# Kernel tuning notes

Hardware: AMD Instinct MI355X
Metric: run time of the kernel (lower is better)

Reference implementation:

```python
import jax, jax.numpy as jnp
import numpy as np

N, M = 20000, 5000
D_IN, D_OUT = 256, 512
EPS = 1e-5


def setup_inputs() -> dict:
    key = jax.random.key(0)
    k1, k2, k3, k4 = jax.random.split(key, 4)
    x = jax.random.normal(k1, (N, D_IN), dtype=jnp.float32)
    H = (jax.random.uniform(k2, (N, M)) < 0.05).astype(jnp.float32)
    W_node = jax.random.normal(k3, (D_IN, D_OUT), dtype=jnp.float32) / np.sqrt(D_IN)
    W_res = jax.random.normal(k4, (D_IN, D_OUT), dtype=jnp.float32) / np.sqrt(D_IN)
    gamma = jnp.ones((D_OUT,), dtype=jnp.float32)
    beta = jnp.zeros((D_OUT,), dtype=jnp.float32)
    return {"x": x, "H": H, "W_node": W_node, "W_res": W_res, "gamma": gamma, "beta": beta}


def reference(x, H, W_node, W_res, gamma, beta):
    # degrees, clamped to >= 1
    d_v = jnp.clip(jnp.sum(H, axis=1), 1.0)   # [N] node degree
    d_e = jnp.clip(jnp.sum(H, axis=0), 1.0)   # [M] hyperedge degree
    x_proj = x @ W_node                       # [N, d_out]
    edge_feat = (H.T @ x_proj) / d_e[:, None] # [M, d_out] node -> edge aggregation
    node_update = (H @ edge_feat) / d_v[:, None]  # [N, d_out] edge -> node
    h = node_update + x @ W_res               # residual (d_in != d_out -> linear)
    # LayerNorm over last dim
    mu = jnp.mean(h, axis=-1, keepdims=True)
    var = jnp.mean(jnp.square(h - mu), axis=-1, keepdims=True)
    out = (h - mu) * jax.lax.rsqrt(var + EPS) * gamma + beta
    return out  # dropout is identity at inference
```

## Files before the change

### kernel.cpp

```cpp
#include <hip/hip_runtime.h>


#define N_NODES 20000
#define M_EDGES 5000
#define MPAD    5120
#define NPAD    20480
#define NW      320
#define MW      80
#define DIN     256
#define DOUT    512
#define SPLITS  16

typedef short bf16x4 __attribute__((ext_vector_type(4)));
typedef short bf16x8 __attribute__((ext_vector_type(8)));
typedef float f32x4 __attribute__((ext_vector_type(4)));
typedef unsigned long long u64;

#define MFMA16(A, B, C) __builtin_amdgcn_mfma_f32_16x16x32_bf16((A), (B), (C), 0, 0, 0)

__device__ __forceinline__ unsigned short f2b(float f) {
  unsigned u = __builtin_bit_cast(unsigned, f);
  return (unsigned short)((u + 0x7FFFu + ((u >> 16) & 1u)) >> 16);
}

__device__ __forceinline__ void stage16(const void* g, void* l) {
  __builtin_amdgcn_global_load_lds(
      (const __attribute__((address_space(1))) unsigned int*)g,
      (__attribute__((address_space(3))) unsigned int*)l, 16, 0, 0);
}

__device__ __forceinline__ bf16x8 expand8(unsigned b) {
  union { unsigned u[4]; bf16x8 v; } r;
  const unsigned t = b | (b << 15);
  r.u[0] = (t & 0x00010001u) * 0x3F80u;
  r.u[1] = ((t >> 2) & 0x00010001u) * 0x3F80u;
  r.u[2] = ((t >> 4) & 0x00010001u) * 0x3F80u;
  r.u[3] = ((t >> 6) & 0x00010001u) * 0x3F80u;
  return r.v;
}

__global__ __launch_bounds__(256) void prep_kernel(const float* __restrict__ Wn,
                                                   const float* __restrict__ Wr,
                                                   unsigned short* __restrict__ WT) {
  const int q = blockIdx.x * 256 + threadIdx.x;
  const int j = q >> 9, k = q & 511;
  const float v = (k < 256) ? Wn[(size_t)k * 512 + j] : Wr[(size_t)(k - 256) * 512 + j];
  WT[(size_t)j * 512 + k] = f2b(v);
}

__global__ __launch_bounds__(256) void xt_kernel(const float* __restrict__ x,
                                                 unsigned short* __restrict__ xpb) {
  const int j = threadIdx.x;
  const int n8 = blockIdx.x;
  union { unsigned u[4]; bf16x8 v; } o;
#pragma unroll
  for (int p = 0; p < 4; ++p) {
    const int n = n8 * 8 + 2 * p;
    const float v0 = (n < N_NODES) ? x[(size_t)n * DIN + j] : 0.f;
    const float v1 = (n + 1 < N_NODES) ? x[(size_t)(n + 1) * DIN + j] : 0.f;
    o.u[p] = (unsigned)f2b(v0) | ((unsigned)f2b(v1) << 16);
  }
  *(bf16x8*)(xpb + ((size_t)n8 * 256 + j) * 8) = o.v;
}

__global__ __launch_bounds__(256) void pack_kernel(const float* __restrict__ H,
                                                   u64* __restrict__ Hb,
                                                   u64* __restrict__ HTb) {
  const int t = threadIdx.x;
  const int l = t & 63;
  const int w = t >> 6;
  const int g = blockIdx.x;
  const int h = blockIdx.y;
  const int n0 = g * 64;
  const int mc = h * 1024 + 4 * t;
  u64 ht0 = 0, ht1 = 0, ht2 = 0, ht3 = 0;
  const int mw = h * 16 + w * 4 + (l >> 4);
  u64* hbp = Hb + (size_t)mw * NPAD + n0;
  const bool hbw = ((l & 15) == 0);
  const int shn = 4 * (l & 15);

  for (int r = 0; r < 64; ++r) {
    const int n = n0 + r;
    unsigned nib = 0;
    if (n < N_NODES) {
      if (mc + 3 < M_EDGES) {
        const float4 v = *(const float4*)(H + (size_t)n * M_EDGES + mc);
        nib = (v.x != 0.f ? 1u : 0u) | (v.y != 0.f ? 2u : 0u) |
              (v.z != 0.f ? 4u : 0u) | (v.w != 0.f ? 8u : 0u);
      } else if (mc < M_EDGES) {
#pragma unroll
        for (int j = 0; j < 4; ++j)
          if (mc + j < M_EDGES)
            nib |= (H[(size_t)n * M_EDGES + mc + j] != 0.f ? 1u : 0u) << j;
      }
    }
    ht0 |= (u64)(nib & 1u) << r;
    ht1 |= (u64)((nib >> 1) & 1u) << r;
    ht2 |= (u64)((nib >> 2) & 1u) << r;
    ht3 |= (u64)((nib >> 3) & 1u) << r;
    u64 val = (u64)nib << shn;
    val |= __shfl_xor(val, 1, 64);
    val |= __shfl_xor(val, 2, 64);
    val |= __shfl_xor(val, 4, 64);
    val |= __shfl_xor(val, 8, 64);
    if (hbw) hbp[r] = val;
  }
  u64* htp = HTb + (size_t)g * MPAD + mc;
  htp[0] = ht0; htp[1] = ht1; htp[2] = ht2; htp[3] = ht3;
}

__global__ __launch_bounds__(256) void deg_kernel(const u64* __restrict__ Hb,
                                                  const u64* __restrict__ HTb,
                                                  float* __restrict__ inv_de,
                                                  float* __restrict__ inv_dv) {
  const int g = blockIdx.x * 256 + threadIdx.x;
  if (g < MPAD) {
    int c = 0;
    for (int nw = 0; nw < NW; ++nw) c += __popcll(HTb[(size_t)nw * MPAD + g]);
    inv_de[g] = 1.f / fmaxf((float)c, 1.f);
  } else if (g < MPAD + NPAD) {
    const int n = g - MPAD;
    int c = 0;
#pragma unroll
    for (int mw = 0; mw < MW; ++mw) c += __popcll(Hb[(size_t)mw * NPAD + n]);
    inv_dv[n] = 1.f / fmaxf((float)c, 1.f);
  }
}

__global__ __launch_bounds__(256) void gemmA_kernel(const unsigned short* __restrict__ xpb,
                                                    const u64* __restrict__ HTb,
                                                    float* __restrict__ partial) {
  __shared__ char lds[2][8192];
  const int t = threadIdx.x;
  const int w = t >> 6, l = t & 63;
  const int lr = l & 15, lg = l >> 4;
  const int shl8 = lg * 8;
  const int wgid = blockIdx.x;
  const int mchunk = wgid >> 6;
  const int sj = wgid & 63;
  const int s = sj >> 2, jb = sj & 3;
  const int m0 = mchunk * 256 + w * 64;
  const int j0 = jb * 64;

  f32x4 acc[4][4] = {};
  const u64* bbase = HTb + (size_t)(s * 20) * MPAD + m0 + lr;
  const char* xb = (const char*)xpb;
  const int n8b = s * 160;
  const int sj0 = j0 + w * 16 + lr;

  u64 b00, b01, b02, b03, b10, b11, b12, b13;

#define GA_LOADB(S, st_) do {                                                  \
    const u64* bp_ = bbase + (size_t)(st_) * MPAD;                             \
    b##S##0 = bp_[0]; b##S##1 = bp_[16]; b##S##2 = bp_[32]; b##S##3 = bp_[48]; \
  } while (0)

#define GA_STAGE(buf, st_) do {                                                \
    const size_t s0_ = ((size_t)(n8b + (st_) * 8 + lg) * 256 + sj0) * 16;      \
    const size_t s1_ = ((size_t)(n8b + (st_) * 8 + 4 + lg) * 256 + sj0) * 16;  \
    stage16(xb + s0_, &lds[buf][w * 1024 + l * 16]);                           \
    stage16(xb + s1_, &lds[buf][(4 + w) * 1024 + l * 16]);                     \
  } while (0)

#define GA_JG(jg, BW) do {                                                     \
    const unsigned wlo_ = (unsigned)(BW), whi_ = (unsigned)((BW) >> 32);       \
    const bf16x8 e0_ = expand8((wlo_ >> shl8) & 255u);                         \
    const bf16x8 e1_ = expand8((whi_ >> shl8) & 255u);                         \
    acc[0][jg] = MFMA16(A00_, e0_, acc[0][jg]);                                \
    acc[1][jg] = MFMA16(A10_, e0_, acc[1][jg]);                                \
    acc[2][jg] = MFMA16(A20_, e0_, acc[2][jg]);                                \
    acc[3][jg] = MFMA16(A30_, e0_, acc[3][jg]);                                \
    acc[0][jg] = MFMA16(A01_, e1_, acc[0][jg]);                                \
    acc[1][jg] = MFMA16(A11_, e1_, acc[1][jg]);                                \
    acc[2][jg] = MFMA16(A21_, e1_, acc[2][jg]);                                \
    acc[3][jg] = MFMA16(A31_, e1_, acc[3][jg]);                                \
  } while (0)

#define GA_COMP(buf, S) do {                                                   \
    const char* L_ = &lds[buf][0];                                             \
    const bf16x8 A00_ = *(const bf16x8*)(L_ + l * 16 + 0);                     \
    const bf16x8 A10_ = *(const bf16x8*)(L_ + l * 16 + 1024);                  \
    const bf16x8 A20_ = *(const bf16x8*)(L_ + l * 16 + 2048);                  \
    const bf16x8 A30_ = *(const bf16x8*)(L_ + l * 16 + 3072);                  \
    const bf16x8 A01_ = *(const bf16x8*)(L_ + l * 16 + 4096);                  \
    const bf16x8 A11_ = *(const bf16x8*)(L_ + l * 16 + 5120);                  \
    const bf16x8 A21_ = *(const bf16x8*)(L_ + l * 16 + 6144);                  \
    const bf16x8 A31_ = *(const bf16x8*)(L_ + l * 16 + 7168);                  \
    GA_JG(0, b##S##0); GA_JG(1, b##S##1); GA_JG(2, b##S##2); GA_JG(3, b##S##3);\
  } while (0)

  GA_LOADB(0, 0);
  GA_STAGE(0, 0);
  for (int st = 0; st < 20; st += 2) {
    const int n1 = (st + 1 < 20) ? st + 1 : 19;
    GA_LOADB(1, n1); GA_STAGE(1, n1);
    asm volatile("s_waitcnt vmcnt(6)" ::: "memory");
    __builtin_amdgcn_s_barrier();
    GA_COMP(0, 0);
    __builtin_amdgcn_s_barrier();
    const int n2 = (st + 2 < 20) ? st + 2 : 19;
    GA_LOADB(0, n2); GA_STAGE(0, n2);
    asm volatile("s_waitcnt vmcnt(6)" ::: "memory");
    __builtin_amdgcn_s_barrier();
    GA_COMP(1, 1);
    __builtin_amdgcn_s_barrier();
  }
#undef GA_LOADB
#undef GA_STAGE
#undef GA_JG
#undef GA_COMP

  float* pp = partial + (size_t)s * (DIN * MPAD);
#pragma unroll
  for (int fr = 0; fr < 4; ++fr)
#pragma unroll
    for (int r = 0; r < 4; ++r) {
      const int j = j0 + fr * 16 + lg * 4 + r;
#pragma unroll
      for (int jg = 0; jg < 4; ++jg)
        pp[(size_t)j * MPAD + m0 + jg * 16 + lr] = acc[fr][jg][r];
    }
}

__global__ __launch_bounds__(256) void reduceA_kernel(const float* __restrict__ partial,
                                                      const float* __restrict__ inv_de,
                                                      unsigned short* __restrict__ t2p) {
  const int t = threadIdx.x;
  const int m = blockIdx.x * 256 + t;
  const int jc = blockIdx.y * 16;
  const float e = inv_de[m];
  unsigned short* ob = t2p + ((size_t)(m >> 3) * 256) * 8 + (m & 7);
  for (int jj = 0; jj < 16; ++jj) {
    const int j = jc + jj;
    const float* p = partial + (size_t)j * MPAD + m;
    float s = 0.f;
#pragma unroll
    for (int sp = 0; sp < SPLITS; ++sp) s += p[(size_t)sp * (DIN * MPAD)];
    ob[(size_t)j * 8] = f2b(s * e);
  }
}

__global__ __launch_bounds__(256) void gemmB_kernel(const unsigned short* __restrict__ t2p,
                                                    const u64* __restrict__ Hb,
                                                    float* __restrict__ partialB) {
  __shared__ char lds[2][8192];
  const int t = threadIdx.x;
  const int w = t >> 6, l = t & 63;
  const int lr = l & 15, lg = l >> 4;
  const int shl8 = lg * 8;
  const int wgid = blockIdx.x;
  const int nchunk = wgid >> 3;
  const int sj = wgid & 7;
  const int s = sj >> 2, jb = sj & 3;
  const int n0 = nchunk * 256 + w * 64;
  const int j0 = jb * 64;

  f32x4 acc[4][4] = {};
  const u64* abase = Hb + (size_t)(s * 40) * NPAD + n0 + lr;
  const char* tb = (const char*)t2p;
  const int m8b = s * 320;
  const int sj0 = j0 + w * 16 + lr;

  u64 a00, a01, a02, a03, a10, a11, a12, a13;

#define GB_LOADA(S, st_) do {                                                  \
    const u64* ap_ = abase + (size_t)(st_) * NPAD;                             \
    a##S##0 = ap_[0]; a##S##1 = ap_[16]; a##S##2 = ap_[32]; a##S##3 = ap_[48]; \
  } while (0)

#define GB_STAGE(buf, st_) do {                                                \
    const size_t s0_ = ((size_t)(m8b + (st_) * 8 + lg) * 256 + sj0) * 16;      \
    const size_t s1_ = ((size_t)(m8b + (st_) * 8 + 4 + lg) * 256 + sj0) * 16;  \
    stage16(tb + s0_, &lds[buf][w * 1024 + l * 16]);                           \
    stage16(tb + s1_, &lds[buf][(4 + w) * 1024 + l * 16]);                     \
  } while (0)

#define GB_FR(fr, AW) do {                                                     \
    const unsigned wlo_ = (unsigned)(AW), whi_ = (unsigned)((AW) >> 32);       \
    const bf16x8 e0_ = expand8((wlo_ >> shl8) & 255u);                         \
    const bf16x8 e1_ = expand8((whi_ >> shl8) & 255u);                         \
    acc[fr][0] = MFMA16(e0_, B00_, acc[fr][0]);                                \
    acc[fr][1] = MFMA16(e0_, B10_, acc[fr][1]);                                \
    acc[fr][2] = MFMA16(e0_, B20_, acc[fr][2]);                                \
    acc[fr][3] = MFMA16(e0_, B30_, acc[fr][3]);                                \
    acc[fr][0] = MFMA16(e1_, B01_, acc[fr][0]);                                \
    acc[fr][1] = MFMA16(e1_, B11_, acc[fr][1]);                                \
    acc[fr][2] = MFMA16(e1_, B21_, acc[fr][2]);                                \
    acc[fr][3] = MFMA16(e1_, B31_, acc[fr][3]);                                \
  } while (0)

#define GB_COMP(buf, S) do {                                                   \
    const char* L_ = &lds[buf][0];                                             \
    const bf16x8 B00_ = *(const bf16x8*)(L_ + l * 16 + 0);                     \
    const bf16x8 B10_ = *(const bf16x8*)(L_ + l * 16 + 1024);                  \
    const bf16x8 B20_ = *(const bf16x8*)(L_ + l * 16 + 2048);                  \
    const bf16x8 B30_ = *(const bf16x8*)(L_ + l * 16 + 3072);                  \
    const bf16x8 B01_ = *(const bf16x8*)(L_ + l * 16 + 4096);                  \
    const bf16x8 B11_ = *(const bf16x8*)(L_ + l * 16 + 5120);                  \
    const bf16x8 B21_ = *(const bf16x8*)(L_ + l * 16 + 6144);                  \
    const bf16x8 B31_ = *(const bf16x8*)(L_ + l * 16 + 7168);                  \
    GB_FR(0, a##S##0); GB_FR(1, a##S##1); GB_FR(2, a##S##2); GB_FR(3, a##S##3);\
  } while (0)

  GB_LOADA(0, 0);
  GB_STAGE(0, 0);
  for (int st = 0; st < 40; st += 2) {
    const int n1 = (st + 1 < 40) ? st + 1 : 39;
    GB_LOADA(1, n1); GB_STAGE(1, n1);
    asm volatile("s_waitcnt vmcnt(6)" ::: "memory");
    __builtin_amdgcn_s_barrier();
    GB_COMP(0, 0);
    __builtin_amdgcn_s_barrier();
    const int n2 = (st + 2 < 40) ? st + 2 : 39;
    GB_LOADA(0, n2); GB_STAGE(0, n2);
    asm volatile("s_waitcnt vmcnt(6)" ::: "memory");
    __builtin_amdgcn_s_barrier();
    GB_COMP(1, 1);
    __builtin_amdgcn_s_barrier();
  }
#undef GB_LOADA
#undef GB_STAGE
#undef GB_FR
#undef GB_COMP

  float* pp = partialB + (size_t)s * ((size_t)NPAD * DIN);
#pragma unroll
  for (int fr = 0; fr < 4; ++fr) {
#pragma unroll
    for (int r = 0; r < 4; ++r) {
      const int n = n0 + fr * 16 + lg * 4 + r;
#pragma unroll
      for (int jg = 0; jg < 4; ++jg)
        pp[(size_t)n * DIN + j0 + jg * 16 + lr] = acc[fr][jg][r];
    }
  }
}

__global__ __launch_bounds__(256) void reduceB_kernel(const float* __restrict__ partialB,
                                                      const float* __restrict__ inv_dv,
                                                      unsigned short* __restrict__ T3) {
  const size_t idx4 = (size_t)blockIdx.x * 1024 + threadIdx.x * 4;
  const f32x4 a = *(const f32x4*)(partialB + idx4);
  const f32x4 b = *(const f32x4*)(partialB + (size_t)NPAD * DIN + idx4);
  const float dv = inv_dv[idx4 >> 8];
  bf16x4 o;
#pragma unroll
  for (int i = 0; i < 4; ++i) o[i] = (short)f2b((a[i] + b[i]) * dv);
  *(bf16x4*)(T3 + idx4) = o;
}

__global__ __launch_bounds__(512) void gemmC_kernel(const float* __restrict__ x,
                                                    const unsigned short* __restrict__ T3,
                                                    const unsigned short* __restrict__ WT,
                                                    float* __restrict__ out) {
  __shared__ unsigned short As[128 * 64];
  __shared__ unsigned short Bsh[128 * 64];
  const int t = threadIdx.x;
  const int n0 = blockIdx.x * 128;
  const int j0 = blockIdx.y * 128;
  const int w = t >> 6, l = t & 63;
  const int wr = w >> 2, wc = w & 3;
  const int lr = l & 15, lg = l >> 4;
  f32x4 acc[4][2];
#pragma unroll
  for (int i = 0; i < 4; ++i)
#pragma unroll
    for (int jq = 0; jq < 2; ++jq) acc[i][jq] = (f32x4){0.f, 0.f, 0.f, 0.f};
  const int sr = t >> 3, sk8 = t & 7;

  for (int st = 0; st < 8; ++st) {
    __syncthreads();
#pragma unroll
    for (int p = 0; p < 2; ++p) {
      const int node = sr + p * 64;
      const int gn = n0 + node;
      bf16x8 pk;
      if (st < 4) {
        if (gn < N_NODES)
          pk = *(const bf16x8*)(T3 + (size_t)gn * DIN + st * 64 + sk8 * 8);
        else {
#pragma unroll
          for (int jq = 0; jq < 8; ++jq) pk[jq] = 0;
        }
      } else {
        if (gn < N_NODES) {
          const float4* p4 = (const float4*)(x + (size_t)gn * DIN + (st - 4) * 64 + sk8 * 8);
          const float4 q0 = p4[0], q1 = p4[1];
          pk[0] = (short)f2b(q0.x); pk[1] = (short)f2b(q0.y); pk[2] = (short)f2b(q0.z); pk[3] = (short)f2b(q0.w);
          pk[4] = (short)f2b(q1.x); pk[5] = (short)f2b(q1.y); pk[6] = (short)f2b(q1.z); pk[7] = (short)f2b(q1.w);
        } else {
#pragma unroll
          for (int jq = 0; jq < 8; ++jq) pk[jq] = 0;
        }
      }
      *(bf16x8*)((char*)As + node * 128 + ((sk8 * 16) ^ ((node & 7) << 4))) = pk;
    }
#pragma unroll
    for (int p = 0; p < 2; ++p) {
      const int j = sr + p * 64;
      const bf16x8 pk = *(const bf16x8*)(WT + (size_t)(j0 + j) * 512 + st * 64 + sk8 * 8);
      *(bf16x8*)((char*)Bsh + j * 128 + ((sk8 * 16) ^ ((j & 7) << 4))) = pk;
    }
    __syncthreads();
#pragma unroll
    for (int ks = 0; ks < 2; ++ks) {
      const int kb = ks * 64 + 16 * lg;
      bf16x8 bf[2];
#pragma unroll
      for (int fc = 0; fc < 2; ++fc) {
        const int row = wc * 32 + fc * 16 + lr;
        bf[fc] = *(const bf16x8*)((const char*)Bsh + row * 128 + (kb ^ ((row & 7) << 4)));
      }
#pragma unroll
      for (int fr = 0; fr < 4; ++fr) {
        const int row = wr * 64 + fr * 16 + lr;
        const bf16x8 af = *(const bf16x8*)((const char*)As + row * 128 + (kb ^ ((row & 7) << 4)));
#pragma unroll
        for (int fc = 0; fc < 2; ++fc)
          acc[fr][fc] = __builtin_amdgcn_mfma_f32_16x16x32_bf16(af, bf[fc], acc[fr][fc], 0, 0, 0);
      }
    }
  }
#pragma unroll
  for (int fr = 0; fr < 4; ++fr)
#pragma unroll
    for (int fc = 0; fc < 2; ++fc) {
      const int col = j0 + wc * 32 + fc * 16 + lr;
#pragma unroll
      for (int r = 0; r < 4; ++r) {
        const int row = n0 + wr * 64 + fr * 16 + 4 * lg + r;
        if (row < N_NODES) out[(size_t)row * DOUT + col] = acc[fr][fc][r];
      }
    }
}

__global__ __launch_bounds__(256) void ln_kernel(float* __restrict__ out,
                                                 const float* __restrict__ gamma,
                                                 const float* __restrict__ beta) {
  const int row = blockIdx.x * 4 + (threadIdx.x >> 6);
  const int l = threadIdx.x & 63;
  float* p = out + (size_t)row * DOUT;
  float4 va = *(const float4*)(p + 4 * l);
  float4 vb = *(const float4*)(p + 256 + 4 * l);
  float s = va.x + va.y + va.z + va.w + vb.x + vb.y + vb.z + vb.w;
  float s2 = va.x * va.x + va.y * va.y + va.z * va.z + va.w * va.w +
             vb.x * vb.x + vb.y * vb.y + vb.z * vb.z + vb.w * vb.w;
#pragma unroll
  for (int m = 1; m < 64; m <<= 1) { s += __shfl_xor(s, m, 64); s2 += __shfl_xor(s2, m, 64); }
  const float mu = s * (1.f / DOUT);
  const float rs = rsqrtf(s2 * (1.f / DOUT) - mu * mu + 1e-5f);
  const float4 g0 = *(const float4*)(gamma + 4 * l);
  const float4 g1 = *(const float4*)(gamma + 256 + 4 * l);
  const float4 b0 = *(const float4*)(beta + 4 * l);
  const float4 b1 = *(const float4*)(beta + 256 + 4 * l);
  va.x = (va.x - mu) * rs * g0.x + b0.x;  va.y = (va.y - mu) * rs * g0.y + b0.y;
  va.z = (va.z - mu) * rs * g0.z + b0.z;  va.w = (va.w - mu) * rs * g0.w + b0.w;
  vb.x = (vb.x - mu) * rs * g1.x + b1.x;  vb.y = (vb.y - mu) * rs * g1.y + b1.y;
  vb.z = (vb.z - mu) * rs * g1.z + b1.z;  vb.w = (vb.w - mu) * rs * g1.w + b1.w;
  *(float4*)(p + 4 * l) = va;
  *(float4*)(p + 256 + 4 * l) = vb;
}

extern "C" void kernel_launch(void* const* d_in, const int* in_sizes, int n_in,
                              void* d_out, int out_size, void* d_ws, size_t ws_size,
                              hipStream_t stream) {
  (void)in_sizes; (void)n_in; (void)out_size; (void)ws_size;
  const float* x = (const float*)d_in[0];
  const float* H = (const float*)d_in[1];
  const float* Wn = (const float*)d_in[2];
  const float* Wr = (const float*)d_in[3];
  const float* gamma = (const float*)d_in[4];
  const float* beta = (const float*)d_in[5];
  float* out = (float*)d_out;
  char* ws = (char*)d_ws;

  unsigned short* WT  = (unsigned short*)(ws + 0);
  u64* Hb             = (u64*)(ws + 524288);
  u64* HTb            = (u64*)(ws + 13631488);
  float* inv_de       = (float*)(ws + 26738688);
  float* inv_dv       = (float*)(ws + 26759168);
  unsigned short* xpb = (unsigned short*)(ws + 26841088);
  float* partialA     = (float*)(ws + 37326848);
  unsigned short* t2p = (unsigned short*)(ws + 121212928);
  float* partialB     = (float*)(ws + 123834368);
  unsigned short* T3  = (unsigned short*)(ws + 165777408);

  prep_kernel<<<dim3(1024), dim3(256), 0, stream>>>(Wn, Wr, WT);
  xt_kernel<<<dim3(2560), dim3(256), 0, stream>>>(x, xpb);
  pack_kernel<<<dim3(320, 5), dim3(256), 0, stream>>>(H, Hb, HTb);
  deg_kernel<<<dim3(100), dim3(256), 0, stream>>>(Hb, HTb, inv_de, inv_dv);
  gemmA_kernel<<<dim3(1280), dim3(256), 0, stream>>>(xpb, HTb, partialA);
  reduceA_kernel<<<dim3(20, 16), dim3(256), 0, stream>>>(partialA, inv_de, t2p);
  gemmB_kernel<<<dim3(640), dim3(256), 0, stream>>>(t2p, Hb, partialB);
  reduceB_kernel<<<dim3(5000), dim3(256), 0, stream>>>(partialB, inv_dv, T3);
  gemmC_kernel<<<dim3(157, 4), dim3(512), 0, stream>>>(x, T3, WT, out);
  ln_kernel<<<dim3(5000), dim3(256), 0, stream>>>(out, gamma, beta);
}
```

Before: 337.1 us.

## Split H packing and transpose, deepen GEMM k-steps, raise gemmB split-K

```diff
diff --git a/kernel.cpp b/kernel.cpp
--- a/kernel.cpp
+++ b/kernel.cpp
@@ -10,6 +10,7 @@
 #define DIN     256
 #define DOUT    512
 #define SPLITS  16
+#define SPLITSB 4
 
 typedef short bf16x4 __attribute__((ext_vector_type(4)));
 typedef short bf16x8 __attribute__((ext_vector_type(8)));
@@ -64,49 +65,52 @@
 }
 
 __global__ __launch_bounds__(256) void pack_kernel(const float* __restrict__ H,
-                                                   u64* __restrict__ Hb,
                                                    u64* __restrict__ HTb) {
   const int t = threadIdx.x;
-  const int l = t & 63;
-  const int w = t >> 6;
   const int g = blockIdx.x;
-  const int h = blockIdx.y;
   const int n0 = g * 64;
-  const int mc = h * 1024 + 4 * t;
-  u64 ht0 = 0, ht1 = 0, ht2 = 0, ht3 = 0;
-  const int mw = h * 16 + w * 4 + (l >> 4);
-  u64* hbp = Hb + (size_t)mw * NPAD + n0;
-  const bool hbw = ((l & 15) == 0);
-  const int shn = 4 * (l & 15);
-
+  u64 ht[20] = {};
+#pragma unroll 2
   for (int r = 0; r < 64; ++r) {
     const int n = n0 + r;
-    unsigned nib = 0;
     if (n < N_NODES) {
-      if (mc + 3 < M_EDGES) {
-        const float4 v = *(const float4*)(H + (size_t)n * M_EDGES + mc);
-        nib = (v.x != 0.f ? 1u : 0u) | (v.y != 0.f ? 2u : 0u) |
-              (v.z != 0.f ? 4u : 0u) | (v.w != 0.f ? 8u : 0u);
-      } else if (mc < M_EDGES) {
-#pragma unroll
-        for (int j = 0; j < 4; ++j)
-          if (mc + j < M_EDGES)
-            nib |= (H[(size_t)n * M_EDGES + mc + j] != 0.f ? 1u : 0u) << j;
+      const float* row = H + (size_t)n * M_EDGES;
+#pragma unroll
+      for (int p = 0; p < 5; ++p) {
+        const int mc = p * 1024 + 4 * t;
+        if (p < 4 || mc + 3 < M_EDGES) {
+          const float4 v = *(const float4*)(row + mc);
+          ht[4 * p + 0] |= (u64)(v.x != 0.f) << r;
+          ht[4 * p + 1] |= (u64)(v.y != 0.f) << r;
+          ht[4 * p + 2] |= (u64)(v.z != 0.f) << r;
+          ht[4 * p + 3] |= (u64)(v.w != 0.f) << r;
+        }
       }
     }
-    ht0 |= (u64)(nib & 1u) << r;
-    ht1 |= (u64)((nib >> 1) & 1u) << r;
-    ht2 |= (u64)((nib >> 2) & 1u) << r;
-    ht3 |= (u64)((nib >> 3) & 1u) << r;
-    u64 val = (u64)nib << shn;
-    val |= __shfl_xor(val, 1, 64);
-    val |= __shfl_xor(val, 2, 64);
-    val |= __shfl_xor(val, 4, 64);
-    val |= __shfl_xor(val, 8, 64);
-    if (hbw) hbp[r] = val;
-  }
-  u64* htp = HTb + (size_t)g * MPAD + mc;
-  htp[0] = ht0; htp[1] = ht1; htp[2] = ht2; htp[3] = ht3;
+  }
+  u64* base = HTb + (size_t)g * MPAD + 4 * t;
+#pragma unroll
+  for (int p = 0; p < 5; ++p) {
+    u64* hp = base + p * 1024;
+    hp[0] = ht[4 * p + 0]; hp[1] = ht[4 * p + 1];
+    hp[2] = ht[4 * p + 2]; hp[3] = ht[4 * p + 3];
+  }
+}
+
+__global__ __launch_bounds__(256) void bt_kernel(const u64* __restrict__ HTb,
+                                                 u64* __restrict__ Hb) {
+  const int t = threadIdx.x;
+  const int w = t >> 6, l = t & 63;
+  const int id = blockIdx.x * 4 + w;
+  const int nw = id % NW;
+  const int mw = id / NW;
+  const u64 word = HTb[(size_t)nw * MPAD + mw * 64 + l];
+  u64 out = 0;
+  for (int r = 0; r < 64; ++r) {
+    const u64 mask = __ballot(((word >> r) & 1ull) != 0);
+    if (l == r) out = mask;
+  }
+  Hb[(size_t)mw * NPAD + nw * 64 + l] = out;
 }
 
 __global__ __launch_bounds__(256) void deg_kernel(const u64* __restrict__ Hb,
@@ -130,7 +134,7 @@
 __global__ __launch_bounds__(256) void gemmA_kernel(const unsigned short* __restrict__ xpb,
                                                     const u64* __restrict__ HTb,
                                                     float* __restrict__ partial) {
-  __shared__ char lds[2][8192];
+  __shared__ char lds[2][16384];
   const int t = threadIdx.x;
   const int w = t >> 6, l = t & 63;
   const int lr = l & 15, lg = l >> 4;
@@ -148,18 +152,22 @@
   const int n8b = s * 160;
   const int sj0 = j0 + w * 16 + lr;
 
-  u64 b00, b01, b02, b03, b10, b11, b12, b13;
+  u64 b00, b01, b02, b03, b04, b05, b06, b07;
+  u64 b10, b11, b12, b13, b14, b15, b16, b17;
 
 #define GA_LOADB(S, st_) do {                                                  \
-    const u64* bp_ = bbase + (size_t)(st_) * MPAD;                             \
+    const u64* bp_ = bbase + (size_t)(st_) * 2 * MPAD;                         \
     b##S##0 = bp_[0]; b##S##1 = bp_[16]; b##S##2 = bp_[32]; b##S##3 = bp_[48]; \
+    const u64* bq_ = bp_ + MPAD;                                               \
+    b##S##4 = bq_[0]; b##S##5 = bq_[16]; b##S##6 = bq_[32]; b##S##7 = bq_[48]; \
   } while (0)
 
 #define GA_STAGE(buf, st_) do {                                                \
-    const size_t s0_ = ((size_t)(n8b + (st_) * 8 + lg) * 256 + sj0) * 16;      \
-    const size_t s1_ = ((size_t)(n8b + (st_) * 8 + 4 + lg) * 256 + sj0) * 16;  \
-    stage16(xb + s0_, &lds[buf][w * 1024 + l * 16]);                           \
-    stage16(xb + s1_, &lds[buf][(4 + w) * 1024 + l * 16]);                     \
+    const size_t r0_ = (size_t)(n8b + (st_) * 16 + lg) * 256 + sj0;            \
+    stage16(xb + (r0_) * 16,              &lds[buf][(w) * 1024 + l * 16]);     \
+    stage16(xb + (r0_ + 4 * 256) * 16,    &lds[buf][(4 + w) * 1024 + l * 16]); \
+    stage16(xb + (r0_ + 8 * 256) * 16,    &lds[buf][(8 + w) * 1024 + l * 16]); \
+    stage16(xb + (r0_ + 12 * 256) * 16,   &lds[buf][(12 + w) * 1024 + l * 16]);\
   } while (0)
 
 #define GA_JG(jg, BW) do {                                                     \
@@ -176,8 +184,8 @@
     acc[3][jg] = MFMA16(A31_, e1_, acc[3][jg]);                                \
   } while (0)
 
-#define GA_COMP(buf, S) do {                                                   \
-    const char* L_ = &lds[buf][0];                                             \
+#define GA_COMP(buf, h, W0, W1, W2, W3) do {                                   \
+    const char* L_ = &lds[buf][(h) * 8192];                                    \
     const bf16x8 A00_ = *(const bf16x8*)(L_ + l * 16 + 0);                     \
     const bf16x8 A10_ = *(const bf16x8*)(L_ + l * 16 + 1024);                  \
     const bf16x8 A20_ = *(const bf16x8*)(L_ + l * 16 + 2048);                  \
@@ -186,23 +194,25 @@
     const bf16x8 A11_ = *(const bf16x8*)(L_ + l * 16 + 5120);                  \
     const bf16x8 A21_ = *(const bf16x8*)(L_ + l * 16 + 6144);                  \
     const bf16x8 A31_ = *(const bf16x8*)(L_ + l * 16 + 7168);                  \
-    GA_JG(0, b##S##0); GA_JG(1, b##S##1); GA_JG(2, b##S##2); GA_JG(3, b##S##3);\
+    GA_JG(0, W0); GA_JG(1, W1); GA_JG(2, W2); GA_JG(3, W3);                    \
   } while (0)
 
   GA_LOADB(0, 0);
   GA_STAGE(0, 0);
-  for (int st = 0; st < 20; st += 2) {
-    const int n1 = (st + 1 < 20) ? st + 1 : 19;
+  for (int st = 0; st < 10; st += 2) {
+    const int n1 = (st + 1 < 10) ? st + 1 : 9;
     GA_LOADB(1, n1); GA_STAGE(1, n1);
-    asm volatile("s_waitcnt vmcnt(6)" ::: "memory");
-    __builtin_amdgcn_s_barrier();
-    GA_COMP(0, 0);
-    __builtin_amdgcn_s_barrier();
-    const int n2 = (st + 2 < 20) ? st + 2 : 19;
+    asm volatile("s_waitcnt vmcnt(12)" ::: "memory");
+    __builtin_amdgcn_s_barrier();
+    GA_COMP(0, 0, b00, b01, b02, b03);
+    GA_COMP(0, 1, b04, b05, b06, b07);
+    __builtin_amdgcn_s_barrier();
+    const int n2 = (st + 2 < 10) ? st + 2 : 9;
     GA_LOADB(0, n2); GA_STAGE(0, n2);
-    asm volatile("s_waitcnt vmcnt(6)" ::: "memory");
-    __builtin_amdgcn_s_barrier();
-    GA_COMP(1, 1);
+    asm volatile("s_waitcnt vmcnt(12)" ::: "memory");
+    __builtin_amdgcn_s_barrier();
+    GA_COMP(1, 0, b10, b11, b12, b13);
+    GA_COMP(1, 1, b14, b15, b16, b17);
     __builtin_amdgcn_s_barrier();
   }
 #undef GA_LOADB
@@ -243,36 +253,40 @@
 __global__ __launch_bounds__(256) void gemmB_kernel(const unsigned short* __restrict__ t2p,
                                                     const u64* __restrict__ Hb,
                                                     float* __restrict__ partialB) {
-  __shared__ char lds[2][8192];
+  __shared__ char lds[2][16384];
   const int t = threadIdx.x;
   const int w = t >> 6, l = t & 63;
   const int lr = l & 15, lg = l >> 4;
   const int shl8 = lg * 8;
   const int wgid = blockIdx.x;
-  const int nchunk = wgid >> 3;
-  const int sj = wgid & 7;
+  const int nchunk = wgid >> 4;
+  const int sj = wgid & 15;
   const int s = sj >> 2, jb = sj & 3;
   const int n0 = nchunk * 256 + w * 64;
   const int j0 = jb * 64;
 
   f32x4 acc[4][4] = {};
-  const u64* abase = Hb + (size_t)(s * 40) * NPAD + n0 + lr;
+  const u64* abase = Hb + (size_t)(s * 20) * NPAD + n0 + lr;
   const char* tb = (const char*)t2p;
-  const int m8b = s * 320;
+  const int m8b = s * 160;
   const int sj0 = j0 + w * 16 + lr;
 
-  u64 a00, a01, a02, a03, a10, a11, a12, a13;
+  u64 a00, a01, a02, a03, a04, a05, a06, a07;
+  u64 a10, a11, a12, a13, a14, a15, a16, a17;
 
 #define GB_LOADA(S, st_) do {                                                  \
-    const u64* ap_ = abase + (size_t)(st_) * NPAD;                             \
+    const u64* ap_ = abase + (size_t)(st_) * 2 * NPAD;                         \
     a##S##0 = ap_[0]; a##S##1 = ap_[16]; a##S##2 = ap_[32]; a##S##3 = ap_[48]; \
+    const u64* aq_ = ap_ + NPAD;                                               \
+    a##S##4 = aq_[0]; a##S##5 = aq_[16]; a##S##6 = aq_[32]; a##S##7 = aq_[48]; \
   } while (0)
 
 #define GB_STAGE(buf, st_) do {                                                \
-    const size_t s0_ = ((size_t)(m8b + (st_) * 8 + lg) * 256 + sj0) * 16;      \
-    const size_t s1_ = ((size_t)(m8b + (st_) * 8 + 4 + lg) * 256 + sj0) * 16;  \
-    stage16(tb + s0_, &lds[buf][w * 1024 + l * 16]);                           \
-    stage16(tb + s1_, &lds[buf][(4 + w) * 1024 + l * 16]);                     \
+    const size_t r0_ = (size_t)(m8b + (st_) * 16 + lg) * 256 + sj0;            \
+    stage16(tb + (r0_) * 16,              &lds[buf][(w) * 1024 + l * 16]);     \
+    stage16(tb + (r0_ + 4 * 256) * 16,    &lds[buf][(4 + w) * 1024 + l * 16]); \
+    stage16(tb + (r0_ + 8 * 256) * 16,    &lds[buf][(8 + w) * 1024 + l * 16]); \
+    stage16(tb + (r0_ + 12 * 256) * 16,   &lds[buf][(12 + w) * 1024 + l * 16]);\
   } while (0)
 
 #define GB_FR(fr, AW) do {                                                     \
@@ -289,8 +303,8 @@
     acc[fr][3] = MFMA16(e1_, B31_, acc[fr][3]);                                \
   } while (0)
 
-#define GB_COMP(buf, S) do {                                                   \
-    const char* L_ = &lds[buf][0];                                             \
+#define GB_COMP(buf, h, W0, W1, W2, W3) do {                                   \
+    const char* L_ = &lds[buf][(h) * 8192];                                    \
     const bf16x8 B00_ = *(const bf16x8*)(L_ + l * 16 + 0);                     \
     const bf16x8 B10_ = *(const bf16x8*)(L_ + l * 16 + 1024);                  \
     const bf16x8 B20_ = *(const bf16x8*)(L_ + l * 16 + 2048);                  \
@@ -299,23 +313,25 @@
     const bf16x8 B11_ = *(const bf16x8*)(L_ + l * 16 + 5120);                  \
     const bf16x8 B21_ = *(const bf16x8*)(L_ + l * 16 + 6144);                  \
     const bf16x8 B31_ = *(const bf16x8*)(L_ + l * 16 + 7168);                  \
-    GB_FR(0, a##S##0); GB_FR(1, a##S##1); GB_FR(2, a##S##2); GB_FR(3, a##S##3);\
+    GB_FR(0, W0); GB_FR(1, W1); GB_FR(2, W2); GB_FR(3, W3);                    \
   } while (0)
 
   GB_LOADA(0, 0);
   GB_STAGE(0, 0);
-  for (int st = 0; st < 40; st += 2) {
-    const int n1 = (st + 1 < 40) ? st + 1 : 39;
+  for (int st = 0; st < 10; st += 2) {
+    const int n1 = (st + 1 < 10) ? st + 1 : 9;
     GB_LOADA(1, n1); GB_STAGE(1, n1);
-    asm volatile("s_waitcnt vmcnt(6)" ::: "memory");
-    __builtin_amdgcn_s_barrier();
-    GB_COMP(0, 0);
-    __builtin_amdgcn_s_barrier();
-    const int n2 = (st + 2 < 40) ? st + 2 : 39;
+    asm volatile("s_waitcnt vmcnt(12)" ::: "memory");
+    __builtin_amdgcn_s_barrier();
+    GB_COMP(0, 0, a00, a01, a02, a03);
+    GB_COMP(0, 1, a04, a05, a06, a07);
+    __builtin_amdgcn_s_barrier();
+    const int n2 = (st + 2 < 10) ? st + 2 : 9;
     GB_LOADA(0, n2); GB_STAGE(0, n2);
-    asm volatile("s_waitcnt vmcnt(6)" ::: "memory");
-    __builtin_amdgcn_s_barrier();
-    GB_COMP(1, 1);
+    asm volatile("s_waitcnt vmcnt(12)" ::: "memory");
+    __builtin_amdgcn_s_barrier();
+    GB_COMP(1, 0, a10, a11, a12, a13);
+    GB_COMP(1, 1, a14, a15, a16, a17);
     __builtin_amdgcn_s_barrier();
   }
 #undef GB_LOADA
@@ -340,12 +356,17 @@
                                                       const float* __restrict__ inv_dv,
                                                       unsigned short* __restrict__ T3) {
   const size_t idx4 = (size_t)blockIdx.x * 1024 + threadIdx.x * 4;
-  const f32x4 a = *(const f32x4*)(partialB + idx4);
-  const f32x4 b = *(const f32x4*)(partialB + (size_t)NPAD * DIN + idx4);
+  f32x4 s = (f32x4){0.f, 0.f, 0.f, 0.f};
+#pragma unroll
+  for (int sp = 0; sp < SPLITSB; ++sp) {
+    const f32x4 a = *(const f32x4*)(partialB + (size_t)sp * ((size_t)NPAD * DIN) + idx4);
+#pragma unroll
+    for (int i = 0; i < 4; ++i) s[i] += a[i];
+  }
   const float dv = inv_dv[idx4 >> 8];
   bf16x4 o;
 #pragma unroll
-  for (int i = 0; i < 4; ++i) o[i] = (short)f2b((a[i] + b[i]) * dv);
+  for (int i = 0; i < 4; ++i) o[i] = (short)f2b(s[i] * dv);
   *(bf16x4*)(T3 + idx4) = o;
 }
 
@@ -483,15 +504,16 @@
   float* partialA     = (float*)(ws + 37326848);
   unsigned short* t2p = (unsigned short*)(ws + 121212928);
   float* partialB     = (float*)(ws + 123834368);
-  unsigned short* T3  = (unsigned short*)(ws + 165777408);
+  unsigned short* T3  = (unsigned short*)(ws + 207720448);
 
   prep_kernel<<<dim3(1024), dim3(256), 0, stream>>>(Wn, Wr, WT);
   xt_kernel<<<dim3(2560), dim3(256), 0, stream>>>(x, xpb);
-  pack_kernel<<<dim3(320, 5), dim3(256), 0, stream>>>(H, Hb, HTb);
+  pack_kernel<<<dim3(320), dim3(256), 0, stream>>>(H, HTb);
+  bt_kernel<<<dim3(6400), dim3(256), 0, stream>>>(HTb, Hb);
   deg_kernel<<<dim3(100), dim3(256), 0, stream>>>(Hb, HTb, inv_de, inv_dv);
   gemmA_kernel<<<dim3(1280), dim3(256), 0, stream>>>(xpb, HTb, partialA);
   reduceA_kernel<<<dim3(20, 16), dim3(256), 0, stream>>>(partialA, inv_de, t2p);
-  gemmB_kernel<<<dim3(640), dim3(256), 0, stream>>>(t2p, Hb, partialB);
+  gemmB_kernel<<<dim3(1280), dim3(256), 0, stream>>>(t2p, Hb, partialB);
   reduceB_kernel<<<dim3(5000), dim3(256), 0, stream>>>(partialB, inv_dv, T3);
   gemmC_kernel<<<dim3(157, 4), dim3(512), 0, stream>>>(x, T3, WT, out);
   ln_kernel<<<dim3(5000), dim3(256), 0, stream>>>(out, gamma, beta);
```

New measurement: 365.0 us. 1.08x slower.
